# Optimization experiments

Measured on AMD Instinct MI355X. Metric: run time of the kernel, lower is better.

Reference implementation:

```python
import jax, jax.numpy as jnp
import numpy as np

D, P, MC = 512, 256, 128   # state dim, obs dim, control dim
H, M, T = 32, 64, 1024     # num filters, Hankel/filter length, horizon
GAMMA = 0.9


def setup_inputs() -> dict:
    rng = np.random.default_rng(0)
    # Stable dynamics: scale spectral radius to 0.95
    A = rng.standard_normal((D, D)).astype(np.float32)
    A *= np.float32(0.95 / np.max(np.abs(np.linalg.eigvals(A))))
    B = (rng.standard_normal((D, MC)) / np.sqrt(D)).astype(np.float32)
    C = (rng.standard_normal((P, D)) / np.sqrt(D)).astype(np.float32)
    # SPD cost matrices
    Q_obs = np.eye(P, dtype=np.float32)
    R = (0.1 * np.eye(MC)).astype(np.float32)
    # LQR-like feedback gain (small, applied to y_obs as in the source)
    K = (0.02 * rng.standard_normal((MC, P))).astype(np.float32)
    # Spectral filters from Hankel matrix: Z_ij = gamma^(i+j+2) * 2/((i+j+2)^3-(i+j+2))
    idx = np.arange(M)
    ij = idx[:, None] + idx[None, :] + 2
    Z = (GAMMA ** ij) * 2.0 / (ij ** 3 - ij)
    w, V = np.linalg.eigh(Z)
    sigma = np.abs(w[-H:])
    phi = V[:, -H:]
    sigma_phi = (sigma ** 0.25)[:, None] * phi.T        # [H, M]
    sigma_phi_M = sigma_phi.astype(np.float32)
    # sum over the inner l-loop of sigma_phi_m (the source sums contributions over l)
    s_m = sigma_phi.sum(axis=1).astype(np.float32)       # [H]
    # Learned controller tensor M_il -> [m_control, H, h, p]
    M_tensor = (0.01 * rng.standard_normal((MC, H, H, P))).astype(np.float32)
    x0 = rng.standard_normal(D).astype(np.float32)
    return {
        "A": jnp.asarray(A), "B": jnp.asarray(B), "C": jnp.asarray(C),
        "Q_obs": jnp.asarray(Q_obs), "R": jnp.asarray(R), "K": jnp.asarray(K),
        "M_tensor": jnp.asarray(M_tensor),
        "sigma_phi_M": jnp.asarray(sigma_phi_M), "s_m": jnp.asarray(s_m),
        "x0": jnp.asarray(x0),
    }


def reference(A, B, C, Q_obs, R, K, M_tensor, sigma_phi_M, s_m, x0):
    h, m = sigma_phi_M.shape          # filters, history window
    mc = B.shape[1]
    p = C.shape[0]

    # CAB[i] = C @ A^i @ B for i = 0..h  (Markov parameters for y_nat)
    def pow_step(Ap, _):
        return Ap @ A, C @ (Ap @ B)
    _, CAB = jax.lax.scan(pow_step, jnp.eye(A.shape[0], dtype=A.dtype), None, length=h + 1)  # [h+1, p, mc]

    # Pre-contract M_tensor with the inner filter weights (sum over j/l):
    # u_pert[c] = sum_{i,k,p'} M2[c,i,p'] * sigma_phi_M[i,k] * y_nat_{t-k}[p']
    M2 = jnp.einsum('cijq,j->ciq', M_tensor, s_m)  # [mc, h, p]

    def step(carry, _):
        x, u_buf, y_buf = carry            # x:[d], u_buf:[h+1,mc] newest-first, y_buf:[m,p] newest-first
        y_obs = C @ x                      # [p]
        # natural observation: strip effect of past controls
        y_nat = y_obs - jnp.einsum('ipc,ic->p', CAB, u_buf)
        y_buf = jnp.concatenate([y_nat[None, :], y_buf[:-1]], axis=0)
        # spectral projection of y_nat history, then contract with learned tensor
        y_proj = sigma_phi_M @ y_buf       # [h, p]
        u_pert = jnp.einsum('ciq,iq->c', M2, y_proj)  # [mc]
        u = -(K @ y_obs) + u_pert
        cost = y_obs @ (Q_obs @ y_obs) + u @ (R @ u)
        u_buf = jnp.concatenate([u[None, :], u_buf[:-1]], axis=0)
        x = A @ x + B @ u
        return (x, u_buf, y_buf), cost

    init = (x0,
            jnp.zeros((h + 1, mc), dtype=x0.dtype),
            jnp.zeros((m, p), dtype=x0.dtype))
    _, costs = jax.lax.scan(step, init, None, length=T)
    return costs  # [T] per-step losses
```

## Files before the change

### kernel.cpp

```cpp
#include <hip/hip_runtime.h>

#define TPB 256
#define MAXJ 48

#define SC_N 128
#define YD0 128
#define YU0 160
#define WD0 167
#define WU0 175
#define DT0 182
#define XP0 198
#define XR0 230
#define U0 246
#define NWG 254
#define NGRP 8
#define GCH 32

__device__ __forceinline__ void cst(float* p, float v) {
  __hip_atomic_store(p, v, __ATOMIC_RELAXED, __HIP_MEMORY_SCOPE_AGENT);
}
__device__ __forceinline__ void cstu(unsigned* p, unsigned v) {
  __hip_atomic_store(p, v, __ATOMIC_RELAXED, __HIP_MEMORY_SCOPE_AGENT);
}
__device__ __forceinline__ unsigned cldu(const unsigned* p) {
  return __hip_atomic_load(p, __ATOMIC_RELAXED, __HIP_MEMORY_SCOPE_AGENT);
}
__device__ __forceinline__ float cld(const float* p) {
  return __hip_atomic_load(p, __ATOMIC_RELAXED, __HIP_MEMORY_SCOPE_AGENT);
}
__device__ __forceinline__ float2 cld2(const float* p) {
  unsigned long long u = __hip_atomic_load(
      reinterpret_cast<const unsigned long long*>(p), __ATOMIC_RELAXED,
      __HIP_MEMORY_SCOPE_AGENT);
  float2 v;
  __builtin_memcpy(&v, &u, 8);
  return v;
}

__device__ __forceinline__ void grid_barrier(unsigned* __restrict__ arr,
                                             unsigned* __restrict__ grp,
                                             int bid, int tid, unsigned phase) {
  asm volatile("s_waitcnt vmcnt(0)" ::: "memory");
  __syncthreads();
  if (tid == 0) cstu(arr + (bid << 5), phase);
  if (bid < NGRP) {
    const int lo = bid * GCH;
    const int n = (NWG - lo < GCH) ? (NWG - lo) : GCH;
    if (tid < n) {
      while (cldu(arr + ((lo + tid) << 5)) < phase) __builtin_amdgcn_s_sleep(1);
    }
    __syncthreads();
    if (tid == 0) cstu(grp + (bid << 5), phase);
  }
  if (tid < NGRP) {
    while (cldu(grp + (tid << 5)) < phase) __builtin_amdgcn_s_sleep(1);
  }
  __atomic_signal_fence(__ATOMIC_SEQ_CST);
  __syncthreads();
}

__device__ void gemm_tile(const float* __restrict__ X, const float* __restrict__ Y,
                          float* __restrict__ Z, int M, int N, int Kd,
                          int mtile, int ntile) {
  __shared__ float Xs[16][65];
  __shared__ float Ys[16][65];
  const int tx = threadIdx.x & 15;
  const int ty = threadIdx.x >> 4;
  const int mbase = mtile * 64;
  const int nbase = ntile * 64;
  float acc[4][4] = {};
  for (int k0 = 0; k0 < Kd; k0 += 16) {
#pragma unroll
    for (int r = 0; r < 4; ++r) {
      int idx = threadIdx.x + 256 * r;
      int mm = idx >> 4, kk = idx & 15;
      int gm = mbase + mm, gk = k0 + kk;
      Xs[kk][mm] = (gm < M && gk < Kd) ? X[(size_t)gm * Kd + gk] : 0.f;
      int nn = idx & 63, k2 = idx >> 6;
      int gn = nbase + nn, gk2 = k0 + k2;
      Ys[k2][nn] = (gk2 < Kd && gn < N) ? Y[(size_t)gk2 * N + gn] : 0.f;
    }
    __syncthreads();
#pragma unroll
    for (int kk = 0; kk < 16; ++kk) {
      float xv[4], yv[4];
#pragma unroll
      for (int a = 0; a < 4; ++a) xv[a] = Xs[kk][ty * 4 + a];
#pragma unroll
      for (int b = 0; b < 4; ++b) yv[b] = Ys[kk][tx * 4 + b];
#pragma unroll
      for (int a = 0; a < 4; ++a)
#pragma unroll
        for (int b = 0; b < 4; ++b) acc[a][b] += xv[a] * yv[b];
    }
    __syncthreads();
  }
#pragma unroll
  for (int a = 0; a < 4; ++a) {
    int gm = mbase + ty * 4 + a;
    if (gm < M) {
#pragma unroll
      for (int b = 0; b < 4; ++b) {
        int gn = nbase + tx * 4 + b;
        if (gn < N) Z[(size_t)gm * N + gn] = acc[a][b];
      }
    }
  }
}

struct JobBatch {
  int n;
  int start[MAXJ + 1];
  int xsel[MAXJ], xoff[MAXJ], ysel[MAXJ], yoff[MAXJ], zoff[MAXJ];
  int M[MAXJ], N[MAXJ], K[MAXJ];
};

__global__ __launch_bounds__(256) void multi_gemm(JobBatch jb,
    const float* __restrict__ A, const float* __restrict__ Bm,
    const float* __restrict__ C, const float* __restrict__ Km,
    float* __restrict__ ws) {
  int b = blockIdx.x;
  int j = 0;
  while (j < jb.n - 1 && b >= jb.start[j + 1]) ++j;
  int rel = b - jb.start[j];
  const float* bases[5] = {ws, A, Bm, C, Km};
  const float* X = bases[jb.xsel[j]] + jb.xoff[j];
  const float* Y = bases[jb.ysel[j]] + jb.yoff[j];
  float* Z = ws + jb.zoff[j];
  int tn = jb.N[j] >> 6;
  gemm_tile(X, Y, Z, jb.M[j], jb.N[j], jb.K[j], rel / tn, rel % tn);
}

__global__ __launch_bounds__(256) void m2_kernel(const float* __restrict__ MT,
    const float* __restrict__ sm, float* __restrict__ M2g) {
  int idx = blockIdx.x * 256 + threadIdx.x;
  if (idx >= 128 * 32 * 256) return;
  int q = idx & 255;
  int ci = idx >> 8;
  const float* base = MT + (size_t)ci * 32 * 256 + q;
  float acc = 0.f;
#pragma unroll
  for (int j = 0; j < 32; ++j) acc += base[j * 256] * sm[j];
  M2g[idx] = acc;
}

__global__ __launch_bounds__(256) void wfir_kernel(const float* __restrict__ M2g,
    const float* __restrict__ Phi, float* __restrict__ W) {
  int idx = blockIdx.x * 256 + threadIdx.x;
  if (idx >= 64 * 32768) return;
  int j = idx >> 15;
  int cq = idx & 32767;
  int c = cq >> 8;
  int q = cq & 255;
  float acc = 0.f;
#pragma unroll
  for (int i = 0; i < 32; ++i)
    acc = fmaf(Phi[(i << 6) | j], M2g[(size_t)(((c << 5) | i) << 8) | q], acc);
  W[idx] = acc;
}

__global__ __launch_bounds__(256) void axpy_acl(const float* __restrict__ A,
    const float* __restrict__ BKC, float* __restrict__ Acl, float* __restrict__ P1) {
  int i = blockIdx.x * 256 + threadIdx.x;
  if (i < 262144) {
    float v = A[i] - BKC[i];
    Acl[i] = v;
    P1[i] = v;
  }
}

__global__ void init_kernel(const float* __restrict__ x0, float* __restrict__ xh,
    float* __restrict__ eh, float* __restrict__ ynh, float* __restrict__ uh0,
    float* __restrict__ dbnd, unsigned* __restrict__ arr,
    unsigned* __restrict__ grp) {
  int i = blockIdx.x * 256 + threadIdx.x;
  int stride = gridDim.x * 256;
  for (int k = i; k < 524288; k += stride) cst(xh + k, 0.f);
  for (int k = i; k < 139264; k += stride) cst(eh + k, 0.f);
  for (int k = i; k < 262144; k += stride) cst(ynh + k, 0.f);
  for (int k = i; k < 8192; k += stride) cst(uh0 + k, 0.f);
  for (int k = i; k < NWG * 32; k += stride) cstu(arr + k, 0u);
  for (int k = i; k < NGRP * 32; k += stride) cstu(grp + k, 0u);
  if (i < 512) cst(dbnd + i, x0[i]);
}

__global__ __launch_bounds__(TPB, 1) void main_kernel(
    const float* __restrict__ B, const float* __restrict__ C,
    const float* __restrict__ x0, const float* __restrict__ Wfir,
    const float* __restrict__ KC, const float* __restrict__ W0C,
    const float* __restrict__ Pp, const float* __restrict__ CAp,
    const float* __restrict__ W0CAp, const float* __restrict__ Rnp,
    const float* __restrict__ AB33p, const float* __restrict__ CAB33p,
    const float* __restrict__ W0CAB33p, const float* __restrict__ A8k,
    float* __restrict__ xh, float* __restrict__ uh0, float* __restrict__ eh,
    float* __restrict__ ynh, float* __restrict__ dbnd,
    unsigned* __restrict__ arr, unsigned* __restrict__ grp) {
  __shared__ float smA[64 * 256];
  __shared__ float smY[8 * 256];
  __shared__ float smV[512];
  __shared__ float smW[8 * 128];
  __shared__ float smVx[8 * 516];
  __shared__ float redsc[4][16];
  const int bid = blockIdx.x;
  const int tid = threadIdx.x;

  if (bid < SC_N) {
    for (int i = tid; i < 16384; i += TPB) {
      int j = i >> 8;
      smA[i] = (j >= 1) ? Wfir[(size_t)j * 32768 + bid * 256 + (i & 255)] : 0.f;
    }
    __syncthreads();
#pragma unroll 1
    for (int ph = 0; ph <= 130; ++ph) {
      if (ph >= 1 && ph < 129) {
        const int Ty = ph * 8 - 8;
        for (int i2 = tid; i2 < 1024; i2 += TPB) {
          float2 v = cld2(ynh + (size_t)Ty * 256 + 2 * i2);
          smY[2 * i2] = v.x;
          smY[2 * i2 + 1] = v.y;
        }
        __syncthreads();
        const int q = tid;
        float yreg[8];
#pragma unroll
        for (int s = 0; s < 8; ++s) yreg[s] = smY[s * 256 + q];
        const int wv = tid >> 6;
        const int lane = tid & 63;
#pragma unroll
        for (int kt = 0; kt < 5; ++kt) {
          const int r0 = 1 + 16 * kt;
          float wreg[23];
#pragma unroll
          for (int i = 0; i < 23; ++i) {
            const int j = r0 - 7 + i;
            wreg[i] = (j >= 1 && j <= 63) ? smA[j * 256 + q] : 0.f;
          }
          float acc[16];
#pragma unroll
          for (int a = 0; a < 16; ++a) acc[a] = 0.f;
#pragma unroll
          for (int a = 0; a < 16; ++a)
#pragma unroll
            for (int s = 0; s < 8; ++s) acc[a] += wreg[a + 7 - s] * yreg[s];
#pragma unroll
          for (int a = 0; a < 16; ++a) {
            float v = acc[a];
            v += __shfl_xor(v, 32);
            v += __shfl_xor(v, 16);
            v += __shfl_xor(v, 8);
            v += __shfl_xor(v, 4);
            v += __shfl_xor(v, 2);
            v += __shfl_xor(v, 1);
            if (lane == 0) redsc[wv][a] = v;
          }
          __syncthreads();
          if (tid < 16) {
            const int r = r0 + tid;
            if (r <= 70) {
              float sum = redsc[0][tid] + redsc[1][tid] + redsc[2][tid] + redsc[3][tid];
              atomicAdd(&eh[(size_t)(Ty + r) * 128 + bid], sum);
            }
          }
          __syncthreads();
        }
      }
      grid_barrier(arr, grp, bid, tid, (unsigned)(ph + 1));
    }
  } else if (bid < YU0) {
    const int r = bid - YD0;
    const int s = r >> 2;
    const int qtr = (r & 3) * 64;
    const int row = qtr + (tid >> 2);
    const int ks = (tid & 3) * 128;
    const float* Mrow = (s == 0) ? C : (CAp + (size_t)(s - 1) * 131072);
    const float4* m4 = (const float4*)(Mrow + (size_t)row * 512 + ks);
#pragma unroll 1
    for (int ph = 0; ph <= 130; ++ph) {
      if (ph < 128) {
        const int T = ph * 8;
        {
          float2 v = cld2(dbnd + (size_t)ph * 512 + 2 * tid);
          smV[2 * tid] = v.x;
          smV[2 * tid + 1] = v.y;
        }
        __syncthreads();
        const float4* v4 = (const float4*)(smV + ks);
        float a = 0.f;
#pragma unroll
        for (int it = 0; it < 32; ++it) {
          float4 mm = m4[it], vv = v4[it];
          a += mm.x * vv.x + mm.y * vv.y + mm.z * vv.z + mm.w * vv.w;
        }
        a += __shfl_down(a, 2);
        a += __shfl_down(a, 1);
        if ((tid & 3) == 0) atomicAdd(&ynh[(size_t)(T + s) * 256 + row], a);
      }
      grid_barrier(arr, grp, bid, tid, (unsigned)(ph + 1));
    }
  } else if (bid < WD0) {
    const int m = bid - YU0;
    const int row = tid;
    const float4* m4 = (const float4*)(CAB33p + (size_t)m * 32768 + (size_t)row * 128);
#pragma unroll 1
    for (int ph = 0; ph <= 130; ++ph) {
      if (ph < 128) {
        const int T = ph * 8;
        for (int i2 = tid; i2 < 512; i2 += TPB) {
          float2 v = cld2(uh0 + (size_t)(64 + T - 33) * 128 + 2 * i2);
          smW[2 * i2] = v.x;
          smW[2 * i2 + 1] = v.y;
        }
        __syncthreads();
        float acc[8];
#pragma unroll
        for (int s = 0; s < 8; ++s) acc[s] = 0.f;
#pragma unroll 4
        for (int it = 0; it < 32; ++it) {
          float4 mm = m4[it];
#pragma unroll
          for (int s = 0; s < 8; ++s) {
            if (s > m) {
              float4 vv = ((const float4*)(smW + (s - m - 1) * 128))[it];
              acc[s] += mm.x * vv.x + mm.y * vv.y + mm.z * vv.z + mm.w * vv.w;
            }
          }
        }
#pragma unroll
        for (int s = 0; s < 8; ++s)
          if (s > m) atomicAdd(&ynh[(size_t)(T + s) * 256 + row], acc[s]);
      }
      grid_barrier(arr, grp, bid, tid, (unsigned)(ph + 1));
    }
  } else if (bid < WU0) {
    const int s = bid - WD0;
    const int row = tid >> 1;
    const int seg = tid & 1;
    const float* Mrow = (s == 0) ? W0C : (W0CAp + (size_t)(s - 1) * 65536);
    const float4* m4 = (const float4*)(Mrow + (size_t)row * 512 + seg * 256);
#pragma unroll 1
    for (int ph = 0; ph <= 130; ++ph) {
      if (ph < 128) {
        const int T = ph * 8;
        {
          float2 v = cld2(dbnd + (size_t)ph * 512 + 2 * tid);
          smV[2 * tid] = v.x;
          smV[2 * tid + 1] = v.y;
        }
        __syncthreads();
        const float4* v4 = (const float4*)(smV + seg * 256);
        float a = 0.f;
#pragma unroll
        for (int it = 0; it < 64; ++it) {
          float4 mm = m4[it], vv = v4[it];
          a += mm.x * vv.x + mm.y * vv.y + mm.z * vv.z + mm.w * vv.w;
        }
        a += __shfl_down(a, 1);
        if (seg == 0) atomicAdd(&eh[(size_t)(T + s) * 128 + row], a);
      }
      grid_barrier(arr, grp, bid, tid, (unsigned)(ph + 1));
    }
  } else if (bid < DT0) {
    const int m = bid - WU0;
    const int row = tid >> 1;
    const int seg = tid & 1;
    const float4* m4 = (const float4*)(W0CAB33p + (size_t)m * 16384 + (size_t)row * 128 + seg * 64);
#pragma unroll 1
    for (int ph = 0; ph <= 130; ++ph) {
      if (ph < 128) {
        const int T = ph * 8;
        for (int i2 = tid; i2 < 512; i2 += TPB) {
          float2 v = cld2(uh0 + (size_t)(64 + T - 33) * 128 + 2 * i2);
          smW[2 * i2] = v.x;
          smW[2 * i2 + 1] = v.y;
        }
        __syncthreads();
        float acc[8];
#pragma unroll
        for (int s = 0; s < 8; ++s) acc[s] = 0.f;
#pragma unroll 4
        for (int it = 0; it < 16; ++it) {
          float4 mm = m4[it];
#pragma unroll
          for (int s = 0; s < 8; ++s) {
            if (s > m) {
              float4 vv = ((const float4*)(smW + (s - m - 1) * 128 + seg * 64))[it];
              acc[s] += mm.x * vv.x + mm.y * vv.y + mm.z * vv.z + mm.w * vv.w;
            }
          }
        }
#pragma unroll
        for (int s = 0; s < 8; ++s) {
          if (s > m) {
            float v = acc[s];
            v += __shfl_down(v, 1);
            if (seg == 0) atomicAdd(&eh[(size_t)(T + s) * 128 + row], v);
          }
        }
      }
      grid_barrier(arr, grp, bid, tid, (unsigned)(ph + 1));
    }
  } else if (bid < XP0) {
    const int g = bid - DT0;
    const int row = g * 32 + (tid >> 3);
    const int l8 = tid & 7;
#pragma unroll 1
    for (int ph = 0; ph <= 130; ++ph) {
      if (ph < 127) {
        const int T = ph * 8;
        {
          float2 v = cld2(dbnd + (size_t)ph * 512 + 2 * tid);
          smV[2 * tid] = v.x;
          smV[2 * tid + 1] = v.y;
        }
        for (int i2 = tid; i2 < 512; i2 += TPB) {
          float2 v = cld2(uh0 + (size_t)(64 + T - 33) * 128 + 2 * i2);
          smW[2 * i2] = v.x;
          smW[2 * i2 + 1] = v.y;
        }
        __syncthreads();
        float a = 0.f;
        {
          const float4* m4 = (const float4*)(A8k + (size_t)row * 512 + l8 * 64);
          const float4* v4 = (const float4*)(smV + l8 * 64);
#pragma unroll
          for (int it = 0; it < 16; ++it) {
            float4 mm = m4[it], vv = v4[it];
            a += mm.x * vv.x + mm.y * vv.y + mm.z * vv.z + mm.w * vv.w;
          }
        }
#pragma unroll
        for (int m = 0; m < 8; ++m) {
          const float4* m4 = (const float4*)(AB33p + (size_t)m * 65536 + (size_t)row * 128 + l8 * 16);
          const float4* v4 = (const float4*)(smW + (7 - m) * 128 + l8 * 16);
#pragma unroll
          for (int it = 0; it < 4; ++it) {
            float4 mm = m4[it], vv = v4[it];
            a += mm.x * vv.x + mm.y * vv.y + mm.z * vv.z + mm.w * vv.w;
          }
        }
        a += __shfl_down(a, 4);
        a += __shfl_down(a, 2);
        a += __shfl_down(a, 1);
        if (l8 == 0) cst(&dbnd[(size_t)(ph + 1) * 512 + row], a);
      }
      grid_barrier(arr, grp, bid, tid, (unsigned)(ph + 1));
    }
  } else if (bid < XR0) {
    const int r = bid - XP0;
    const int s = r >> 2;
    const int qtr = (r & 3) << 7;
    const int row = qtr + (tid >> 1);
    const int seg = tid & 1;
#pragma unroll 1
    for (int ph = 0; ph <= 130; ++ph) {
      if (ph >= 2 && ph < 130) {
        const int Tq = ph * 8 - 16;
        {
          const float* src = (ph == 2) ? x0 : (xh + (size_t)(Tq - 1) * 512);
          float2 v = cld2(src + 2 * tid);
          smV[2 * tid] = v.x;
          smV[2 * tid + 1] = v.y;
        }
        __syncthreads();
        const int pslot = (ph == 2) ? s : (s + 1);
        if (pslot == 0) {
          if (seg == 0) atomicAdd(&xh[(size_t)Tq * 512 + row], smV[row]);
        } else {
          const float4* m4 = (const float4*)(Pp + (size_t)(pslot - 1) * 262144 +
                                             (size_t)row * 512 + seg * 256);
          const float4* v4 = (const float4*)(smV + seg * 256);
          float a = 0.f;
#pragma unroll
          for (int it = 0; it < 64; ++it) {
            float4 mm = m4[it], vv = v4[it];
            a += mm.x * vv.x + mm.y * vv.y + mm.z * vv.z + mm.w * vv.w;
          }
          a += __shfl_down(a, 1);
          if (seg == 0) atomicAdd(&xh[(size_t)(Tq + s) * 512 + row], a);
        }
      }
      grid_barrier(arr, grp, bid, tid, (unsigned)(ph + 1));
    }
  } else if (bid < U0) {
    const int r = bid - XR0;
    const int i = r >> 1;
    const int half = (r & 1) << 8;
    const int row = half + tid;
    const float* Rrow = (i == 0) ? (B + (size_t)row * 128)
                                 : (Rnp + (size_t)(i - 1) * 65536 + (size_t)row * 128);
    const float4* m4 = (const float4*)Rrow;
#pragma unroll 1
    for (int ph = 0; ph <= 130; ++ph) {
      if (ph >= 2 && ph < 130) {
        const int Tq = ph * 8 - 16;
        for (int i2 = tid; i2 < 512; i2 += TPB) {
          int idx = 2 * i2;
          float2 v;
          if (ph == 2 && idx < 128) {
            v.x = 0.f;
            v.y = 0.f;
          } else {
            v = cld2(eh + (size_t)(Tq - 1) * 128 + idx);
          }
          smW[idx] = v.x;
          smW[idx + 1] = v.y;
        }
        __syncthreads();
        float acc[8];
#pragma unroll
        for (int s = 0; s < 8; ++s) acc[s] = 0.f;
#pragma unroll 4
        for (int it = 0; it < 32; ++it) {
          float4 mm = m4[it];
#pragma unroll
          for (int s = 0; s < 8; ++s) {
            if (s >= i) {
              float4 vv = ((const float4*)(smW + (s - i) * 128))[it];
              acc[s] += mm.x * vv.x + mm.y * vv.y + mm.z * vv.z + mm.w * vv.w;
            }
          }
        }
#pragma unroll
        for (int s = 0; s < 8; ++s)
          if (s >= i) atomicAdd(&xh[(size_t)(Tq + s) * 512 + row], acc[s]);
      }
      grid_barrier(arr, grp, bid, tid, (unsigned)(ph + 1));
    }
  } else {
    const int g = bid - U0;
    const int o = tid >> 1;
    const int par = tid & 1;
    const int s = o >> 4;
    const int lr = o & 15;
    const int row = g * 16 + lr;
    const float4* m4 = (const float4*)(KC + (size_t)row * 512 + par * 256);
#pragma unroll 1
    for (int ph = 0; ph <= 130; ++ph) {
      if (ph >= 3) {
        const int Tu = ph * 8 - 24;
        for (int i2 = tid; i2 < 2048; i2 += TPB) {
          int idx = 2 * i2;
          int rr = idx >> 9;
          int cc = idx & 511;
          float2 v = cld2(xh + (size_t)(Tu + rr) * 512 + cc);
          smVx[rr * 516 + cc] = v.x;
          smVx[rr * 516 + cc + 1] = v.y;
        }
        __syncthreads();
        const float4* v4 = (const float4*)(smVx + s * 516 + par * 256);
        float a = 0.f;
#pragma unroll
        for (int it = 0; it < 64; ++it) {
          float4 mm = m4[it], vv = v4[it];
          a += mm.x * vv.x + mm.y * vv.y + mm.z * vv.z + mm.w * vv.w;
        }
        a += __shfl_down(a, 1);
        if (par == 0) {
          float u = cld(&eh[(size_t)(Tu + s) * 128 + row]) - a;
          cst(&uh0[(size_t)(64 + Tu + s) * 128 + row], u);
        }
      }
      grid_barrier(arr, grp, bid, tid, (unsigned)(ph + 1));
    }
  }
}

__global__ __launch_bounds__(256) void cost_kernel(const float* __restrict__ C,
    const float* __restrict__ Q, const float* __restrict__ R,
    const float* __restrict__ xh, const float* __restrict__ uh0,
    float* __restrict__ out) {
  __shared__ float xs[512];
  __shared__ float ys[256];
  __shared__ float us[128];
  __shared__ float redw[4];
  const int t = blockIdx.x;
  const int tid = threadIdx.x;
  {
    float2 v = cld2(xh + (size_t)t * 512 + 2 * tid);
    xs[2 * tid] = v.x;
    xs[2 * tid + 1] = v.y;
  }
  if (tid < 64) {
    float2 v = cld2(uh0 + (size_t)(64 + t) * 128 + 2 * tid);
    us[2 * tid] = v.x;
    us[2 * tid + 1] = v.y;
  }
  __syncthreads();
  {
    const float4* m4 = (const float4*)(C + (size_t)tid * 512);
    const float4* v4 = (const float4*)xs;
    float a = 0.f;
    for (int it = 0; it < 128; ++it) {
      float4 mm = m4[it], vv = v4[it];
      a += mm.x * vv.x + mm.y * vv.y + mm.z * vv.z + mm.w * vv.w;
    }
    ys[tid] = a;
  }
  __syncthreads();
  float acc;
  {
    const float* Qr = Q + (size_t)tid * 256;
    float qy = 0.f;
    for (int k = 0; k < 256; ++k) qy = fmaf(Qr[k], ys[k], qy);
    acc = qy * ys[tid];
  }
  if (tid < 128) {
    const float* Rr = R + (size_t)tid * 128;
    float ru = 0.f;
    for (int k = 0; k < 128; ++k) ru = fmaf(Rr[k], us[k], ru);
    acc += ru * us[tid];
  }
  float v = acc;
  v += __shfl_xor(v, 32);
  v += __shfl_xor(v, 16);
  v += __shfl_xor(v, 8);
  v += __shfl_xor(v, 4);
  v += __shfl_xor(v, 2);
  v += __shfl_xor(v, 1);
  if ((tid & 63) == 0) redw[tid >> 6] = v;
  __syncthreads();
  if (tid == 0) out[t] = redw[0] + redw[1] + redw[2] + redw[3];
}

extern "C" void kernel_launch(void* const* d_in, const int* in_sizes, int n_in,
                              void* d_out, int out_size, void* d_ws, size_t ws_size,
                              hipStream_t stream) {
  (void)in_sizes; (void)n_in; (void)out_size; (void)ws_size;
  const float* A = (const float*)d_in[0];
  const float* B = (const float*)d_in[1];
  const float* C = (const float*)d_in[2];
  const float* Q = (const float*)d_in[3];
  const float* R = (const float*)d_in[4];
  const float* Km = (const float*)d_in[5];
  const float* MT = (const float*)d_in[6];
  const float* Phi = (const float*)d_in[7];
  const float* sm = (const float*)d_in[8];
  const float* x0 = (const float*)d_in[9];

  float* ws = (float*)d_ws;
  const int oWfir = 0;
  const int oKC = 2097152;
  const int oW0C = 2162688;
  const int oAcl = 2228224;
  const int oP = 2490368;
  const int oCA = 4587520;
  const int oW0CA = 5505024;
  const int oRn = 5963776;
  const int oApB = 6422528;
  const int oAB33 = 6946816;
  const int oCAB33 = 7471104;
  const int oW0CAB33 = 7700480;
  const int oA2 = 7815168;
  const int oA4 = 8077312;
  const int oA8 = 8339456;
  const int oA16 = 8601600;
  const int oA32 = 8863744;
  const int oM2 = 9125888;
  const int oBKC = oM2;
  const int oxh = 10174464;
  const int ouh0 = 10698752;
  const int oeh = 10838016;
  const int oynh = 10977280;
  const int odbnd = 11239424;
  const int oarr = 11306496;
  const int ogrp = oarr + NWG * 32;

  float* xh = ws + oxh;
  float* uh0 = ws + ouh0;
  float* eh = ws + oeh;
  float* ynh = ws + oynh;
  float* dbnd = ws + odbnd;
  unsigned* arr = (unsigned*)(ws + oarr);
  unsigned* grp = (unsigned*)(ws + ogrp);

  JobBatch jb;
  jb.n = 0;
  jb.start[0] = 0;
  auto J = [&](int xs_, int xo, int ys_, int yo, int zo, int M, int N, int K) {
    int i = jb.n++;
    jb.xsel[i] = xs_; jb.xoff[i] = xo; jb.ysel[i] = ys_; jb.yoff[i] = yo;
    jb.zoff[i] = zo; jb.M[i] = M; jb.N[i] = N; jb.K[i] = K;
    jb.start[i + 1] = jb.start[i] + (M >> 6) * (N >> 6);
  };
  auto L = [&]() {
    multi_gemm<<<dim3(jb.start[jb.n]), dim3(256), 0, stream>>>(jb, A, B, C, Km, ws);
    jb.n = 0;
    jb.start[0] = 0;
  };

  init_kernel<<<dim3(2048), dim3(256), 0, stream>>>(x0, xh, eh, ynh, uh0, dbnd,
                                                    arr, grp);
  m2_kernel<<<dim3(4096), dim3(256), 0, stream>>>(MT, sm, ws + oM2);
  wfir_kernel<<<dim3(8192), dim3(256), 0, stream>>>(ws + oM2, Phi, ws + oWfir);

  J(4, 0, 3, 0, oKC, 128, 512, 256);
  J(1, 0, 1, 0, oA2, 512, 512, 512);
  J(1, 0, 2, 0, oApB, 512, 128, 512);
  J(3, 0, 1, 0, oCA, 256, 512, 512);
  L();
  J(2, 0, 0, oKC, oBKC, 512, 512, 128);
  J(0, oA2, 0, oA2, oA4, 512, 512, 512);
  J(0, oCA, 1, 0, oCA + 131072, 256, 512, 512);
  J(1, 0, 0, oApB, oApB + 65536, 512, 128, 512);
  J(0, oWfir, 3, 0, oW0C, 128, 512, 256);
  L();
  axpy_acl<<<dim3(1024), dim3(256), 0, stream>>>(A, ws + oBKC, ws + oAcl, ws + oP);
  J(0, oA4, 0, oA4, oA8, 512, 512, 512);
  J(0, oP, 0, oP, oP + 262144, 512, 512, 512);
  J(0, oCA, 0, oA2, oCA + 2 * 131072, 256, 512, 512);
  J(0, oCA + 131072, 0, oA2, oCA + 3 * 131072, 256, 512, 512);
  J(0, oW0C, 1, 0, oW0CA, 128, 512, 512);
  J(0, oW0C, 0, oA2, oW0CA + 65536, 128, 512, 512);
  J(0, oA2, 0, oApB, oApB + 2 * 65536, 512, 128, 512);
  J(0, oA2, 0, oApB + 65536, oApB + 3 * 65536, 512, 128, 512);
  L();
  J(0, oA8, 0, oA8, oA16, 512, 512, 512);
  J(0, oP, 0, oP + 262144, oP + 2 * 262144, 512, 512, 512);
  J(0, oP + 262144, 0, oP + 262144, oP + 3 * 262144, 512, 512, 512);
  for (int i = 1; i <= 3; ++i)
    J(0, oCA + (i - 1) * 131072, 0, oA4, oCA + (i + 3) * 131072, 256, 512, 512);
  for (int i = 1; i <= 2; ++i)
    J(0, oW0CA + (i - 1) * 65536, 0, oA2, oW0CA + (i + 1) * 65536, 128, 512, 512);
  for (int k = 1; k <= 4; ++k)
    J(0, oA4, 0, oApB + (k - 1) * 65536, oApB + (k + 3) * 65536, 512, 128, 512);
  J(0, oP, 2, 0, oRn, 512, 128, 512);
  J(0, oP + 262144, 2, 0, oRn + 65536, 512, 128, 512);
  L();
  J(0, oA16, 0, oA16, oA32, 512, 512, 512);
  for (int i = 1; i <= 4; ++i)
    J(0, oP + (i - 1) * 262144, 0, oP + 3 * 262144, oP + (i + 3) * 262144, 512, 512, 512);
  for (int i = 1; i <= 3; ++i)
    J(0, oW0CA + (i - 1) * 65536, 0, oA4, oW0CA + (i + 3) * 65536, 128, 512, 512);
  J(0, oP + 2 * 262144, 2, 0, oRn + 2 * 65536, 512, 128, 512);
  J(0, oP + 3 * 262144, 2, 0, oRn + 3 * 65536, 512, 128, 512);
  L();
  for (int m = 0; m <= 7; ++m)
    J(0, oA32, 0, oApB + m * 65536, oAB33 + m * 65536, 512, 128, 512);
  for (int i = 5; i <= 7; ++i)
    J(0, oP + (i - 1) * 262144, 2, 0, oRn + (i - 1) * 65536, 512, 128, 512);
  L();
  for (int m = 0; m <= 6; ++m)
    J(3, 0, 0, oAB33 + m * 65536, oCAB33 + m * 32768, 256, 128, 512);
  for (int m = 0; m <= 6; ++m)
    J(0, oW0C, 0, oAB33 + m * 65536, oW0CAB33 + m * 16384, 128, 128, 512);
  L();

  main_kernel<<<dim3(NWG), dim3(TPB), 0, stream>>>(
      B, C, x0, ws + oWfir, ws + oKC, ws + oW0C, ws + oP, ws + oCA,
      ws + oW0CA, ws + oRn, ws + oAB33, ws + oCAB33, ws + oW0CAB33,
      ws + oA8, xh, uh0, eh, ynh, dbnd, arr, grp);

  cost_kernel<<<dim3(1024), dim3(256), 0, stream>>>(C, Q, R, xh, uh0,
                                                    (float*)d_out);
}
```

Before: 3.358 ms.

## Replace global grid barrier with per-role dataflow flag waits

Removes the hierarchical all-workgroup grid barrier that ran after every phase. Each role group now publishes its own per-workgroup phase flag and waits only on the specific producer groups (and phase lags) it depends on. This lets independent roles run ahead and cuts the cost of full-grid synchronization across the 131 phases. The risk is correctness: any missed dependency, or a write-after-read hazard that the global barrier used to cover, could now cause a race.

Result: faster. 3.210 ms (-4.4%).

```diff
diff --git a/kernel.cpp b/kernel.cpp
--- a/kernel.cpp
+++ b/kernel.cpp
@@ -13,8 +13,6 @@
 #define XR0 230
 #define U0 246
 #define NWG 254
-#define NGRP 8
-#define GCH 32
 
 __device__ __forceinline__ void cst(float* p, float v) {
   __hip_atomic_store(p, v, __ATOMIC_RELAXED, __HIP_MEMORY_SCOPE_AGENT);
@@ -37,27 +35,27 @@
   return v;
 }
 
-__device__ __forceinline__ void grid_barrier(unsigned* __restrict__ arr,
-                                             unsigned* __restrict__ grp,
-                                             int bid, int tid, unsigned phase) {
-  asm volatile("s_waitcnt vmcnt(0)" ::: "memory");
-  __syncthreads();
-  if (tid == 0) cstu(arr + (bid << 5), phase);
-  if (bid < NGRP) {
-    const int lo = bid * GCH;
-    const int n = (NWG - lo < GCH) ? (NWG - lo) : GCH;
-    if (tid < n) {
-      while (cldu(arr + ((lo + tid) << 5)) < phase) __builtin_amdgcn_s_sleep(1);
-    }
-    __syncthreads();
-    if (tid == 0) cstu(grp + (bid << 5), phase);
-  }
-  if (tid < NGRP) {
-    while (cldu(grp + (tid << 5)) < phase) __builtin_amdgcn_s_sleep(1);
-  }
-  __atomic_signal_fence(__ATOMIC_SEQ_CST);
-  __syncthreads();
-}
+__device__ __forceinline__ void waitr(unsigned* __restrict__ arr, int lo, int n,
+                                      int v, int tid, int laneBase) {
+  if (v <= 0) return;
+  int idx = tid - laneBase;
+  if (idx >= 0 && idx < n) {
+    while (cldu(arr + ((lo + idx) << 5)) < (unsigned)v) __builtin_amdgcn_s_sleep(1);
+  }
+}
+
+#define SETFLAG(ph)                                              \
+  do {                                                           \
+    asm volatile("s_waitcnt vmcnt(0)" ::: "memory");             \
+    __syncthreads();                                             \
+    if (tid == 0) cstu(arr + (bid << 5), (unsigned)((ph) + 1));  \
+  } while (0)
+
+#define WAITSYNC()                            \
+  do {                                        \
+    __atomic_signal_fence(__ATOMIC_SEQ_CST);  \
+    __syncthreads();                          \
+  } while (0)
 
 __device__ void gemm_tile(const float* __restrict__ X, const float* __restrict__ Y,
                           float* __restrict__ Z, int M, int N, int Kd,
@@ -171,8 +169,7 @@
 
 __global__ void init_kernel(const float* __restrict__ x0, float* __restrict__ xh,
     float* __restrict__ eh, float* __restrict__ ynh, float* __restrict__ uh0,
-    float* __restrict__ dbnd, unsigned* __restrict__ arr,
-    unsigned* __restrict__ grp) {
+    float* __restrict__ dbnd, unsigned* __restrict__ arr) {
   int i = blockIdx.x * 256 + threadIdx.x;
   int stride = gridDim.x * 256;
   for (int k = i; k < 524288; k += stride) cst(xh + k, 0.f);
@@ -180,7 +177,6 @@
   for (int k = i; k < 262144; k += stride) cst(ynh + k, 0.f);
   for (int k = i; k < 8192; k += stride) cst(uh0 + k, 0.f);
   for (int k = i; k < NWG * 32; k += stride) cstu(arr + k, 0u);
-  for (int k = i; k < NGRP * 32; k += stride) cstu(grp + k, 0u);
   if (i < 512) cst(dbnd + i, x0[i]);
 }
 
@@ -194,7 +190,7 @@
     const float* __restrict__ W0CAB33p, const float* __restrict__ A8k,
     float* __restrict__ xh, float* __restrict__ uh0, float* __restrict__ eh,
     float* __restrict__ ynh, float* __restrict__ dbnd,
-    unsigned* __restrict__ arr, unsigned* __restrict__ grp) {
+    unsigned* __restrict__ arr) {
   __shared__ float smA[64 * 256];
   __shared__ float smY[8 * 256];
   __shared__ float smV[512];
@@ -211,60 +207,61 @@
     }
     __syncthreads();
 #pragma unroll 1
-    for (int ph = 0; ph <= 130; ++ph) {
-      if (ph >= 1 && ph < 129) {
-        const int Ty = ph * 8 - 8;
-        for (int i2 = tid; i2 < 1024; i2 += TPB) {
-          float2 v = cld2(ynh + (size_t)Ty * 256 + 2 * i2);
-          smY[2 * i2] = v.x;
-          smY[2 * i2 + 1] = v.y;
+    for (int ph = 1; ph <= 128; ++ph) {
+      waitr(arr, YD0, 32, ph, tid, 0);
+      waitr(arr, YU0, 7, ph, tid, 32);
+      WAITSYNC();
+      const int Ty = ph * 8 - 8;
+      for (int i2 = tid; i2 < 1024; i2 += TPB) {
+        float2 v = cld2(ynh + (size_t)Ty * 256 + 2 * i2);
+        smY[2 * i2] = v.x;
+        smY[2 * i2 + 1] = v.y;
+      }
+      __syncthreads();
+      const int q = tid;
+      float yreg[8];
+#pragma unroll
+      for (int s = 0; s < 8; ++s) yreg[s] = smY[s * 256 + q];
+      const int wv = tid >> 6;
+      const int lane = tid & 63;
+#pragma unroll
+      for (int kt = 0; kt < 5; ++kt) {
+        const int r0 = 1 + 16 * kt;
+        float wreg[23];
+#pragma unroll
+        for (int i = 0; i < 23; ++i) {
+          const int j = r0 - 7 + i;
+          wreg[i] = (j >= 1 && j <= 63) ? smA[j * 256 + q] : 0.f;
+        }
+        float acc[16];
+#pragma unroll
+        for (int a = 0; a < 16; ++a) acc[a] = 0.f;
+#pragma unroll
+        for (int a = 0; a < 16; ++a)
+#pragma unroll
+          for (int s = 0; s < 8; ++s) acc[a] += wreg[a + 7 - s] * yreg[s];
+#pragma unroll
+        for (int a = 0; a < 16; ++a) {
+          float v = acc[a];
+          v += __shfl_xor(v, 32);
+          v += __shfl_xor(v, 16);
+          v += __shfl_xor(v, 8);
+          v += __shfl_xor(v, 4);
+          v += __shfl_xor(v, 2);
+          v += __shfl_xor(v, 1);
+          if (lane == 0) redsc[wv][a] = v;
         }
         __syncthreads();
-        const int q = tid;
-        float yreg[8];
-#pragma unroll
-        for (int s = 0; s < 8; ++s) yreg[s] = smY[s * 256 + q];
-        const int wv = tid >> 6;
-        const int lane = tid & 63;
-#pragma unroll
-        for (int kt = 0; kt < 5; ++kt) {
-          const int r0 = 1 + 16 * kt;
-          float wreg[23];
-#pragma unroll
-          for (int i = 0; i < 23; ++i) {
-            const int j = r0 - 7 + i;
-            wreg[i] = (j >= 1 && j <= 63) ? smA[j * 256 + q] : 0.f;
+        if (tid < 16) {
+          const int r = r0 + tid;
+          if (r <= 70) {
+            float sum = redsc[0][tid] + redsc[1][tid] + redsc[2][tid] + redsc[3][tid];
+            atomicAdd(&eh[(size_t)(Ty + r) * 128 + bid], sum);
           }
-          float acc[16];
-#pragma unroll
-          for (int a = 0; a < 16; ++a) acc[a] = 0.f;
-#pragma unroll
-          for (int a = 0; a < 16; ++a)
-#pragma unroll
-            for (int s = 0; s < 8; ++s) acc[a] += wreg[a + 7 - s] * yreg[s];
-#pragma unroll
-          for (int a = 0; a < 16; ++a) {
-            float v = acc[a];
-            v += __shfl_xor(v, 32);
-            v += __shfl_xor(v, 16);
-            v += __shfl_xor(v, 8);
-            v += __shfl_xor(v, 4);
-            v += __shfl_xor(v, 2);
-            v += __shfl_xor(v, 1);
-            if (lane == 0) redsc[wv][a] = v;
-          }
-          __syncthreads();
-          if (tid < 16) {
-            const int r = r0 + tid;
-            if (r <= 70) {
-              float sum = redsc[0][tid] + redsc[1][tid] + redsc[2][tid] + redsc[3][tid];
-              atomicAdd(&eh[(size_t)(Ty + r) * 128 + bid], sum);
-            }
-          }
-          __syncthreads();
-        }
-      }
-      grid_barrier(arr, grp, bid, tid, (unsigned)(ph + 1));
+        }
+        __syncthreads();
+      }
+      SETFLAG(ph);
     }
   } else if (bid < YU0) {
     const int r = bid - YD0;
@@ -275,61 +272,61 @@
     const float* Mrow = (s == 0) ? C : (CAp + (size_t)(s - 1) * 131072);
     const float4* m4 = (const float4*)(Mrow + (size_t)row * 512 + ks);
 #pragma unroll 1
-    for (int ph = 0; ph <= 130; ++ph) {
-      if (ph < 128) {
-        const int T = ph * 8;
-        {
-          float2 v = cld2(dbnd + (size_t)ph * 512 + 2 * tid);
-          smV[2 * tid] = v.x;
-          smV[2 * tid + 1] = v.y;
-        }
-        __syncthreads();
-        const float4* v4 = (const float4*)(smV + ks);
-        float a = 0.f;
-#pragma unroll
-        for (int it = 0; it < 32; ++it) {
-          float4 mm = m4[it], vv = v4[it];
-          a += mm.x * vv.x + mm.y * vv.y + mm.z * vv.z + mm.w * vv.w;
-        }
-        a += __shfl_down(a, 2);
-        a += __shfl_down(a, 1);
-        if ((tid & 3) == 0) atomicAdd(&ynh[(size_t)(T + s) * 256 + row], a);
-      }
-      grid_barrier(arr, grp, bid, tid, (unsigned)(ph + 1));
+    for (int ph = 0; ph < 128; ++ph) {
+      waitr(arr, DT0, 16, ph, tid, 0);
+      WAITSYNC();
+      const int T = ph * 8;
+      {
+        float2 v = cld2(dbnd + (size_t)ph * 512 + 2 * tid);
+        smV[2 * tid] = v.x;
+        smV[2 * tid + 1] = v.y;
+      }
+      __syncthreads();
+      const float4* v4 = (const float4*)(smV + ks);
+      float a = 0.f;
+#pragma unroll
+      for (int it = 0; it < 32; ++it) {
+        float4 mm = m4[it], vv = v4[it];
+        a += mm.x * vv.x + mm.y * vv.y + mm.z * vv.z + mm.w * vv.w;
+      }
+      a += __shfl_down(a, 2);
+      a += __shfl_down(a, 1);
+      if ((tid & 3) == 0) atomicAdd(&ynh[(size_t)(T + s) * 256 + row], a);
+      SETFLAG(ph);
     }
   } else if (bid < WD0) {
     const int m = bid - YU0;
     const int row = tid;
     const float4* m4 = (const float4*)(CAB33p + (size_t)m * 32768 + (size_t)row * 128);
 #pragma unroll 1
-    for (int ph = 0; ph <= 130; ++ph) {
-      if (ph < 128) {
-        const int T = ph * 8;
-        for (int i2 = tid; i2 < 512; i2 += TPB) {
-          float2 v = cld2(uh0 + (size_t)(64 + T - 33) * 128 + 2 * i2);
-          smW[2 * i2] = v.x;
-          smW[2 * i2 + 1] = v.y;
-        }
-        __syncthreads();
-        float acc[8];
-#pragma unroll
-        for (int s = 0; s < 8; ++s) acc[s] = 0.f;
+    for (int ph = 0; ph < 128; ++ph) {
+      waitr(arr, U0, 8, (ph >= 4 ? ph : 0), tid, 0);
+      WAITSYNC();
+      const int T = ph * 8;
+      for (int i2 = tid; i2 < 512; i2 += TPB) {
+        float2 v = cld2(uh0 + (size_t)(64 + T - 33) * 128 + 2 * i2);
+        smW[2 * i2] = v.x;
+        smW[2 * i2 + 1] = v.y;
+      }
+      __syncthreads();
+      float acc[8];
+#pragma unroll
+      for (int s = 0; s < 8; ++s) acc[s] = 0.f;
 #pragma unroll 4
-        for (int it = 0; it < 32; ++it) {
-          float4 mm = m4[it];
-#pragma unroll
-          for (int s = 0; s < 8; ++s) {
-            if (s > m) {
-              float4 vv = ((const float4*)(smW + (s - m - 1) * 128))[it];
-              acc[s] += mm.x * vv.x + mm.y * vv.y + mm.z * vv.z + mm.w * vv.w;
-            }
+      for (int it = 0; it < 32; ++it) {
+        float4 mm = m4[it];
+#pragma unroll
+        for (int s = 0; s < 8; ++s) {
+          if (s > m) {
+            float4 vv = ((const float4*)(smW + (s - m - 1) * 128))[it];
+            acc[s] += mm.x * vv.x + mm.y * vv.y + mm.z * vv.z + mm.w * vv.w;
           }
         }
-#pragma unroll
-        for (int s = 0; s < 8; ++s)
-          if (s > m) atomicAdd(&ynh[(size_t)(T + s) * 256 + row], acc[s]);
-      }
-      grid_barrier(arr, grp, bid, tid, (unsigned)(ph + 1));
+      }
+#pragma unroll
+      for (int s = 0; s < 8; ++s)
+        if (s > m) atomicAdd(&ynh[(size_t)(T + s) * 256 + row], acc[s]);
+      SETFLAG(ph);
     }
   } else if (bid < WU0) {
     const int s = bid - WD0;
@@ -338,26 +335,26 @@
     const float* Mrow = (s == 0) ? W0C : (W0CAp + (size_t)(s - 1) * 65536);
     const float4* m4 = (const float4*)(Mrow + (size_t)row * 512 + seg * 256);
 #pragma unroll 1
-    for (int ph = 0; ph <= 130; ++ph) {
-      if (ph < 128) {
-        const int T = ph * 8;
-        {
-          float2 v = cld2(dbnd + (size_t)ph * 512 + 2 * tid);
-          smV[2 * tid] = v.x;
-          smV[2 * tid + 1] = v.y;
-        }
-        __syncthreads();
-        const float4* v4 = (const float4*)(smV + seg * 256);
-        float a = 0.f;
-#pragma unroll
-        for (int it = 0; it < 64; ++it) {
-          float4 mm = m4[it], vv = v4[it];
-          a += mm.x * vv.x + mm.y * vv.y + mm.z * vv.z + mm.w * vv.w;
-        }
-        a += __shfl_down(a, 1);
-        if (seg == 0) atomicAdd(&eh[(size_t)(T + s) * 128 + row], a);
-      }
-      grid_barrier(arr, grp, bid, tid, (unsigned)(ph + 1));
+    for (int ph = 0; ph < 128; ++ph) {
+      waitr(arr, DT0, 16, ph, tid, 0);
+      WAITSYNC();
+      const int T = ph * 8;
+      {
+        float2 v = cld2(dbnd + (size_t)ph * 512 + 2 * tid);
+        smV[2 * tid] = v.x;
+        smV[2 * tid + 1] = v.y;
+      }
+      __syncthreads();
+      const float4* v4 = (const float4*)(smV + seg * 256);
+      float a = 0.f;
+#pragma unroll
+      for (int it = 0; it < 64; ++it) {
+        float4 mm = m4[it], vv = v4[it];
+        a += mm.x * vv.x + mm.y * vv.y + mm.z * vv.z + mm.w * vv.w;
+      }
+      a += __shfl_down(a, 1);
+      if (seg == 0) atomicAdd(&eh[(size_t)(T + s) * 128 + row], a);
+      SETFLAG(ph);
     }
   } else if (bid < DT0) {
     const int m = bid - WU0;
@@ -365,85 +362,86 @@
     const int seg = tid & 1;
     const float4* m4 = (const float4*)(W0CAB33p + (size_t)m * 16384 + (size_t)row * 128 + seg * 64);
 #pragma unroll 1
-    for (int ph = 0; ph <= 130; ++ph) {
-      if (ph < 128) {
-        const int T = ph * 8;
-        for (int i2 = tid; i2 < 512; i2 += TPB) {
-          float2 v = cld2(uh0 + (size_t)(64 + T - 33) * 128 + 2 * i2);
-          smW[2 * i2] = v.x;
-          smW[2 * i2 + 1] = v.y;
-        }
-        __syncthreads();
-        float acc[8];
-#pragma unroll
-        for (int s = 0; s < 8; ++s) acc[s] = 0.f;
+    for (int ph = 0; ph < 128; ++ph) {
+      waitr(arr, U0, 8, (ph >= 4 ? ph : 0), tid, 0);
+      WAITSYNC();
+      const int T = ph * 8;
+      for (int i2 = tid; i2 < 512; i2 += TPB) {
+        float2 v = cld2(uh0 + (size_t)(64 + T - 33) * 128 + 2 * i2);
+        smW[2 * i2] = v.x;
+        smW[2 * i2 + 1] = v.y;
+      }
+      __syncthreads();
+      float acc[8];
+#pragma unroll
+      for (int s = 0; s < 8; ++s) acc[s] = 0.f;
 #pragma unroll 4
-        for (int it = 0; it < 16; ++it) {
-          float4 mm = m4[it];
-#pragma unroll
-          for (int s = 0; s < 8; ++s) {
-            if (s > m) {
-              float4 vv = ((const float4*)(smW + (s - m - 1) * 128 + seg * 64))[it];
-              acc[s] += mm.x * vv.x + mm.y * vv.y + mm.z * vv.z + mm.w * vv.w;
-            }
-          }
-        }
+      for (int it = 0; it < 16; ++it) {
+        float4 mm = m4[it];
 #pragma unroll
         for (int s = 0; s < 8; ++s) {
           if (s > m) {
-            float v = acc[s];
-            v += __shfl_down(v, 1);
-            if (seg == 0) atomicAdd(&eh[(size_t)(T + s) * 128 + row], v);
+            float4 vv = ((const float4*)(smW + (s - m - 1) * 128 + seg * 64))[it];
+            acc[s] += mm.x * vv.x + mm.y * vv.y + mm.z * vv.z + mm.w * vv.w;
           }
         }
       }
-      grid_barrier(arr, grp, bid, tid, (unsigned)(ph + 1));
+#pragma unroll
+      for (int s = 0; s < 8; ++s) {
+        if (s > m) {
+          float v = acc[s];
+          v += __shfl_down(v, 1);
+          if (seg == 0) atomicAdd(&eh[(size_t)(T + s) * 128 + row], v);
+        }
+      }
+      SETFLAG(ph);
     }
   } else if (bid < XP0) {
     const int g = bid - DT0;
     const int row = g * 32 + (tid >> 3);
     const int l8 = tid & 7;
 #pragma unroll 1
-    for (int ph = 0; ph <= 130; ++ph) {
-      if (ph < 127) {
-        const int T = ph * 8;
-        {
-          float2 v = cld2(dbnd + (size_t)ph * 512 + 2 * tid);
-          smV[2 * tid] = v.x;
-          smV[2 * tid + 1] = v.y;
-        }
-        for (int i2 = tid; i2 < 512; i2 += TPB) {
-          float2 v = cld2(uh0 + (size_t)(64 + T - 33) * 128 + 2 * i2);
-          smW[2 * i2] = v.x;
-          smW[2 * i2 + 1] = v.y;
-        }
-        __syncthreads();
-        float a = 0.f;
-        {
-          const float4* m4 = (const float4*)(A8k + (size_t)row * 512 + l8 * 64);
-          const float4* v4 = (const float4*)(smV + l8 * 64);
-#pragma unroll
-          for (int it = 0; it < 16; ++it) {
-            float4 mm = m4[it], vv = v4[it];
-            a += mm.x * vv.x + mm.y * vv.y + mm.z * vv.z + mm.w * vv.w;
-          }
-        }
-#pragma unroll
-        for (int m = 0; m < 8; ++m) {
-          const float4* m4 = (const float4*)(AB33p + (size_t)m * 65536 + (size_t)row * 128 + l8 * 16);
-          const float4* v4 = (const float4*)(smW + (7 - m) * 128 + l8 * 16);
-#pragma unroll
-          for (int it = 0; it < 4; ++it) {
-            float4 mm = m4[it], vv = v4[it];
-            a += mm.x * vv.x + mm.y * vv.y + mm.z * vv.z + mm.w * vv.w;
-          }
-        }
-        a += __shfl_down(a, 4);
-        a += __shfl_down(a, 2);
-        a += __shfl_down(a, 1);
-        if (l8 == 0) cst(&dbnd[(size_t)(ph + 1) * 512 + row], a);
-      }
-      grid_barrier(arr, grp, bid, tid, (unsigned)(ph + 1));
+    for (int ph = 0; ph <= 126; ++ph) {
+      waitr(arr, DT0, 16, ph, tid, 0);
+      waitr(arr, U0, 8, (ph >= 4 ? ph : 0), tid, 16);
+      WAITSYNC();
+      const int T = ph * 8;
+      {
+        float2 v = cld2(dbnd + (size_t)ph * 512 + 2 * tid);
+        smV[2 * tid] = v.x;
+        smV[2 * tid + 1] = v.y;
+      }
+      for (int i2 = tid; i2 < 512; i2 += TPB) {
+        float2 v = cld2(uh0 + (size_t)(64 + T - 33) * 128 + 2 * i2);
+        smW[2 * i2] = v.x;
+        smW[2 * i2 + 1] = v.y;
+      }
+      __syncthreads();
+      float a = 0.f;
+      {
+        const float4* m4 = (const float4*)(A8k + (size_t)row * 512 + l8 * 64);
+        const float4* v4 = (const float4*)(smV + l8 * 64);
+#pragma unroll
+        for (int it = 0; it < 16; ++it) {
+          float4 mm = m4[it], vv = v4[it];
+          a += mm.x * vv.x + mm.y * vv.y + mm.z * vv.z + mm.w * vv.w;
+        }
+      }
+#pragma unroll
+      for (int m = 0; m < 8; ++m) {
+        const float4* m4 = (const float4*)(AB33p + (size_t)m * 65536 + (size_t)row * 128 + l8 * 16);
+        const float4* v4 = (const float4*)(smW + (7 - m) * 128 + l8 * 16);
+#pragma unroll
+        for (int it = 0; it < 4; ++it) {
+          float4 mm = m4[it], vv = v4[it];
+          a += mm.x * vv.x + mm.y * vv.y + mm.z * vv.z + mm.w * vv.w;
+        }
+      }
+      a += __shfl_down(a, 4);
+      a += __shfl_down(a, 2);
+      a += __shfl_down(a, 1);
+      if (l8 == 0) cst(&dbnd[(size_t)(ph + 1) * 512 + row], a);
+      SETFLAG(ph);
     }
   } else if (bid < XR0) {
     const int r = bid - XP0;
@@ -452,34 +450,35 @@
     const int row = qtr + (tid >> 1);
     const int seg = tid & 1;
 #pragma unroll 1
-    for (int ph = 0; ph <= 130; ++ph) {
-      if (ph >= 2 && ph < 130) {
-        const int Tq = ph * 8 - 16;
-        {
-          const float* src = (ph == 2) ? x0 : (xh + (size_t)(Tq - 1) * 512);
-          float2 v = cld2(src + 2 * tid);
-          smV[2 * tid] = v.x;
-          smV[2 * tid + 1] = v.y;
-        }
-        __syncthreads();
-        const int pslot = (ph == 2) ? s : (s + 1);
-        if (pslot == 0) {
-          if (seg == 0) atomicAdd(&xh[(size_t)Tq * 512 + row], smV[row]);
-        } else {
-          const float4* m4 = (const float4*)(Pp + (size_t)(pslot - 1) * 262144 +
-                                             (size_t)row * 512 + seg * 256);
-          const float4* v4 = (const float4*)(smV + seg * 256);
-          float a = 0.f;
-#pragma unroll
-          for (int it = 0; it < 64; ++it) {
-            float4 mm = m4[it], vv = v4[it];
-            a += mm.x * vv.x + mm.y * vv.y + mm.z * vv.z + mm.w * vv.w;
-          }
-          a += __shfl_down(a, 1);
-          if (seg == 0) atomicAdd(&xh[(size_t)(Tq + s) * 512 + row], a);
-        }
-      }
-      grid_barrier(arr, grp, bid, tid, (unsigned)(ph + 1));
+    for (int ph = 2; ph <= 129; ++ph) {
+      waitr(arr, XP0, 32, (ph >= 3 ? ph : 0), tid, 0);
+      waitr(arr, XR0, 16, (ph >= 3 ? ph : 0), tid, 32);
+      WAITSYNC();
+      const int Tq = ph * 8 - 16;
+      {
+        const float* src = (ph == 2) ? x0 : (xh + (size_t)(Tq - 1) * 512);
+        float2 v = cld2(src + 2 * tid);
+        smV[2 * tid] = v.x;
+        smV[2 * tid + 1] = v.y;
+      }
+      __syncthreads();
+      const int pslot = (ph == 2) ? s : (s + 1);
+      if (pslot == 0) {
+        if (seg == 0) atomicAdd(&xh[(size_t)Tq * 512 + row], smV[row]);
+      } else {
+        const float4* m4 = (const float4*)(Pp + (size_t)(pslot - 1) * 262144 +
+                                           (size_t)row * 512 + seg * 256);
+        const float4* v4 = (const float4*)(smV + seg * 256);
+        float a = 0.f;
+#pragma unroll
+        for (int it = 0; it < 64; ++it) {
+          float4 mm = m4[it], vv = v4[it];
+          a += mm.x * vv.x + mm.y * vv.y + mm.z * vv.z + mm.w * vv.w;
+        }
+        a += __shfl_down(a, 1);
+        if (seg == 0) atomicAdd(&xh[(size_t)(Tq + s) * 512 + row], a);
+      }
+      SETFLAG(ph);
     }
   } else if (bid < U0) {
     const int r = bid - XR0;
@@ -490,41 +489,43 @@
                                  : (Rnp + (size_t)(i - 1) * 65536 + (size_t)row * 128);
     const float4* m4 = (const float4*)Rrow;
 #pragma unroll 1
-    for (int ph = 0; ph <= 130; ++ph) {
-      if (ph >= 2 && ph < 130) {
-        const int Tq = ph * 8 - 16;
-        for (int i2 = tid; i2 < 512; i2 += TPB) {
-          int idx = 2 * i2;
-          float2 v;
-          if (ph == 2 && idx < 128) {
-            v.x = 0.f;
-            v.y = 0.f;
-          } else {
-            v = cld2(eh + (size_t)(Tq - 1) * 128 + idx);
+    for (int ph = 2; ph <= 129; ++ph) {
+      waitr(arr, 0, SC_N, ph, tid, 0);
+      waitr(arr, WD0, 8, ph - 1, tid, 128);
+      waitr(arr, WU0, 7, ph - 1, tid, 136);
+      WAITSYNC();
+      const int Tq = ph * 8 - 16;
+      for (int i2 = tid; i2 < 512; i2 += TPB) {
+        int idx = 2 * i2;
+        float2 v;
+        if (ph == 2 && idx < 128) {
+          v.x = 0.f;
+          v.y = 0.f;
+        } else {
+          v = cld2(eh + (size_t)(Tq - 1) * 128 + idx);
+        }
+        smW[idx] = v.x;
+        smW[idx + 1] = v.y;
+      }
+      __syncthreads();
+      float acc[8];
+#pragma unroll
+      for (int s = 0; s < 8; ++s) acc[s] = 0.f;
+#pragma unroll 4
+      for (int it = 0; it < 32; ++it) {
+        float4 mm = m4[it];
+#pragma unroll
+        for (int s = 0; s < 8; ++s) {
+          if (s >= i) {
+            float4 vv = ((const float4*)(smW + (s - i) * 128))[it];
+            acc[s] += mm.x * vv.x + mm.y * vv.y + mm.z * vv.z + mm.w * vv.w;
           }
-          smW[idx] = v.x;
-          smW[idx + 1] = v.y;
-        }
-        __syncthreads();
-        float acc[8];
-#pragma unroll
-        for (int s = 0; s < 8; ++s) acc[s] = 0.f;
-#pragma unroll 4
-        for (int it = 0; it < 32; ++it) {
-          float4 mm = m4[it];
-#pragma unroll
-          for (int s = 0; s < 8; ++s) {
-            if (s >= i) {
-              float4 vv = ((const float4*)(smW + (s - i) * 128))[it];
-              acc[s] += mm.x * vv.x + mm.y * vv.y + mm.z * vv.z + mm.w * vv.w;
-            }
-          }
-        }
-#pragma unroll
-        for (int s = 0; s < 8; ++s)
-          if (s >= i) atomicAdd(&xh[(size_t)(Tq + s) * 512 + row], acc[s]);
-      }
-      grid_barrier(arr, grp, bid, tid, (unsigned)(ph + 1));
+        }
+      }
+#pragma unroll
+      for (int s = 0; s < 8; ++s)
+        if (s >= i) atomicAdd(&xh[(size_t)(Tq + s) * 512 + row], acc[s]);
+      SETFLAG(ph);
     }
   } else {
     const int g = bid - U0;
@@ -535,32 +536,36 @@
     const int row = g * 16 + lr;
     const float4* m4 = (const float4*)(KC + (size_t)row * 512 + par * 256);
 #pragma unroll 1
-    for (int ph = 0; ph <= 130; ++ph) {
-      if (ph >= 3) {
-        const int Tu = ph * 8 - 24;
-        for (int i2 = tid; i2 < 2048; i2 += TPB) {
-          int idx = 2 * i2;
-          int rr = idx >> 9;
-          int cc = idx & 511;
-          float2 v = cld2(xh + (size_t)(Tu + rr) * 512 + cc);
-          smVx[rr * 516 + cc] = v.x;
-          smVx[rr * 516 + cc + 1] = v.y;
-        }
-        __syncthreads();
-        const float4* v4 = (const float4*)(smVx + s * 516 + par * 256);
-        float a = 0.f;
-#pragma unroll
-        for (int it = 0; it < 64; ++it) {
-          float4 mm = m4[it], vv = v4[it];
-          a += mm.x * vv.x + mm.y * vv.y + mm.z * vv.z + mm.w * vv.w;
-        }
-        a += __shfl_down(a, 1);
-        if (par == 0) {
-          float u = cld(&eh[(size_t)(Tu + s) * 128 + row]) - a;
-          cst(&uh0[(size_t)(64 + Tu + s) * 128 + row], u);
-        }
-      }
-      grid_barrier(arr, grp, bid, tid, (unsigned)(ph + 1));
+    for (int ph = 3; ph <= 130; ++ph) {
+      waitr(arr, XP0, 32, ph, tid, 0);
+      waitr(arr, XR0, 16, ph, tid, 32);
+      waitr(arr, 0, SC_N, ph - 1, tid, 48);
+      waitr(arr, WD0, 8, ph - 2, tid, 176);
+      waitr(arr, WU0, 7, ph - 2, tid, 184);
+      WAITSYNC();
+      const int Tu = ph * 8 - 24;
+      for (int i2 = tid; i2 < 2048; i2 += TPB) {
+        int idx = 2 * i2;
+        int rr = idx >> 9;
+        int cc = idx & 511;
+        float2 v = cld2(xh + (size_t)(Tu + rr) * 512 + cc);
+        smVx[rr * 516 + cc] = v.x;
+        smVx[rr * 516 + cc + 1] = v.y;
+      }
+      __syncthreads();
+      const float4* v4 = (const float4*)(smVx + s * 516 + par * 256);
+      float a = 0.f;
+#pragma unroll
+      for (int it = 0; it < 64; ++it) {
+        float4 mm = m4[it], vv = v4[it];
+        a += mm.x * vv.x + mm.y * vv.y + mm.z * vv.z + mm.w * vv.w;
+      }
+      a += __shfl_down(a, 1);
+      if (par == 0) {
+        float u = cld(&eh[(size_t)(Tu + s) * 128 + row]) - a;
+        cst(&uh0[(size_t)(64 + Tu + s) * 128 + row], u);
+      }
+      SETFLAG(ph);
     }
   }
 }
@@ -663,7 +668,6 @@
   const int oynh = 10977280;
   const int odbnd = 11239424;
   const int oarr = 11306496;
-  const int ogrp = oarr + NWG * 32;
 
   float* xh = ws + oxh;
   float* uh0 = ws + ouh0;
@@ -671,7 +675,6 @@
   float* ynh = ws + oynh;
   float* dbnd = ws + odbnd;
   unsigned* arr = (unsigned*)(ws + oarr);
-  unsigned* grp = (unsigned*)(ws + ogrp);
 
   JobBatch jb;
   jb.n = 0;
@@ -689,7 +692,7 @@
   };
 
   init_kernel<<<dim3(2048), dim3(256), 0, stream>>>(x0, xh, eh, ynh, uh0, dbnd,
-                                                    arr, grp);
+                                                    arr);
   m2_kernel<<<dim3(4096), dim3(256), 0, stream>>>(MT, sm, ws + oM2);
   wfir_kernel<<<dim3(8192), dim3(256), 0, stream>>>(ws + oM2, Phi, ws + oWfir);
 
@@ -748,7 +751,7 @@
   main_kernel<<<dim3(NWG), dim3(TPB), 0, stream>>>(
       B, C, x0, ws + oWfir, ws + oKC, ws + oW0C, ws + oP, ws + oCA,
       ws + oW0CA, ws + oRn, ws + oAB33, ws + oCAB33, ws + oW0CAB33,
-      ws + oA8, xh, uh0, eh, ynh, dbnd, arr, grp);
+      ws + oA8, xh, uh0, eh, ynh, dbnd, arr);
 
   cost_kernel<<<dim3(1024), dim3(256), 0, stream>>>(C, Q, R, xh, uh0,
                                                     (float*)d_out);
```
